# Performance work log

Hardware: AMD Instinct MI355X
Metric: run time of the kernel (lower is better)

Reference implementation:

```python
import jax, jax.numpy as jnp
import numpy as np
from jax import lax

T = 5        # unrolled ISTA iterations (module default)
LAM = 0.1    # soft-threshold level (module default)
B, L, K = 4096, 4096, 128


def _conv1d_same(x, k):
    """TF-style SAME cross-correlation. x: [B, L], k: [K] -> [B, L]."""
    Kw = k.shape[0]
    pad_left = (Kw - 1) // 2
    pad_right = Kw - 1 - pad_left
    out = lax.conv_general_dilated(
        x[:, None, :],            # [B, 1, L]
        k[None, None, :],         # [O=1, I=1, K]
        window_strides=(1,),
        padding=[(pad_left, pad_right)],
        dimension_numbers=("NCH", "OIH", "NCH"),
    )
    return out[:, 0, :]


def setup_inputs() -> dict:
    key = jax.random.key(0)
    k1, k2 = jax.random.split(key)
    y = jax.random.normal(k1, (B, L), dtype=jnp.float32)
    thz_pulse = jax.random.normal(k2, (K,), dtype=jnp.float32)  # learned pulse (trainable)
    step_size = jnp.full((1,), 0.1, dtype=jnp.float32)          # learned step (trainable)
    return {"y": y, "thz_pulse": thz_pulse, "step_size": step_size}


def reference(y, thz_pulse, step_size):
    x = jnp.zeros_like(y)
    h = thz_pulse           # matched-filter kernel
    h_rev = thz_pulse[::-1] # time-reversed kernel (adjoint / correlation)
    s = step_size[0]
    for _ in range(T):
        conv_out = _conv1d_same(y, h)           # H y
        residual = y - conv_out                 # y - H y
        update = _conv1d_same(residual, h_rev)  # H^T residual
        x = x + s * update                      # gradient step
        x = jnp.sign(x) * jax.nn.relu(jnp.abs(x) - LAM)  # soft-threshold
    return x
```

## Files before the change

### kernel.cpp

```cpp
#include <hip/hip_runtime.h>


typedef __bf16 bf16;
typedef __bf16 bf16x4 __attribute__((ext_vector_type(4)));
typedef __bf16 bf16x8 __attribute__((ext_vector_type(8)));
typedef float f32x4 __attribute__((ext_vector_type(4)));

#define LAM 0.1f
#define RPITCH 1028
#define LDSB (16 * RPITCH * 4)
#define WS_AG 0
#define WS_ZERO 80
#define WS_A1 8192
#define WS_A2 12288
#define PYE 360
#define PRE 216

__global__ __launch_bounds__(256) void ista_prep(const float* __restrict__ h,
                                                 bf16* __restrict__ ws) {
  __shared__ float hs[256];
  __shared__ float acp[256];
  __shared__ bf16 gp[384];
  const int tid = threadIdx.x;
  hs[tid] = (tid < 128) ? h[tid] : 0.f;
  gp[tid] = (bf16)0.f;
  if (tid < 128) gp[256 + tid] = (bf16)0.f;
  __syncthreads();
  const int tau = tid & 127;
  {
    const int m0 = (tid >> 7) * 64;
    float p0 = 0.f, p1 = 0.f, p2 = 0.f, p3 = 0.f;
    for (int m = m0; m < m0 + 64; m += 4) {
      p0 += hs[m] * hs[m + tau];     p1 += hs[m + 1] * hs[m + 1 + tau];
      p2 += hs[m + 2] * hs[m + 2 + tau]; p3 += hs[m + 3] * hs[m + 3 + tau];
    }
    acp[tid] = (p0 + p1) + (p2 + p3);
  }
  __syncthreads();
  if (tid < 128) {
    float ac = acp[tid] + acp[tid + 128];
    float g1 = (tau <= 63) ? hs[63 - tau] : 0.f;
    gp[145 + tau] = (bf16)(g1 - ac);
    if (tau > 0) {
      float g2 = (tau <= 64) ? hs[63 + tau] : 0.f;
      gp[145 - tau] = (bf16)(g2 - ac);
    }
  }
  __syncthreads();
  for (int i = tid; i < 1024; i += 256) {
    const int l = i >> 4, dd = i & 15;
    if (dd < 9) {
      const int o = 144 + (l >> 4) * 8 - (l & 15) + (dd - 4) * 32;
      bf16x8 a;
#pragma unroll
      for (int j = 0; j < 8; ++j) a[j] = gp[o + j];
      *reinterpret_cast<bf16x8*>(ws + WS_AG + l * 128 + dd * 8) = a;
    }
  }
  if (tid < 8) ws[WS_ZERO + tid] = (bf16)0.f;
  for (int i = tid; i < 512; i += 256) {
    const int l = i >> 3, dd = i & 7;
    if (dd < 5) {
      const int o = 127 + (l >> 4) * 8 - (l & 15) + (dd - 2) * 32;
      bf16x8 a1, a2;
#pragma unroll
      for (int j = 0; j < 8; ++j) {
        int p = o + j;
        int i1 = p - 64;
        a1[j] = ((unsigned)i1 < 128u) ? (bf16)hs[i1] : (bf16)0.f;
        int i2 = 191 - p;
        a2[j] = ((unsigned)i2 < 128u) ? (bf16)(-hs[i2]) : (bf16)0.f;
      }
      *reinterpret_cast<bf16x8*>(ws + WS_A1 + l * 64 + dd * 8) = a1;
      *reinterpret_cast<bf16x8*>(ws + WS_A2 + l * 64 + dd * 8) = a2;
    }
  }
}

__device__ __forceinline__ void async_copy16(const float* src, void* lds_dst) {
  __builtin_amdgcn_global_load_lds(
      (const __attribute__((address_space(1))) void*)src,
      (__attribute__((address_space(3))) void*)lds_dst, 16, 0, 0);
}

__device__ __forceinline__ bf16x8 load_frag(const float* __restrict__ yl,
                                            int c) {
  float4 v0 = *reinterpret_cast<const float4*>(yl + c);
  float4 v1 = *reinterpret_cast<const float4*>(yl + c + 4);
  bf16x8 b;
  b[0] = (bf16)v0.x; b[1] = (bf16)v0.y; b[2] = (bf16)v0.z; b[3] = (bf16)v0.w;
  b[4] = (bf16)v1.x; b[5] = (bf16)v1.y; b[6] = (bf16)v1.z; b[7] = (bf16)v1.w;
  return b;
}

__global__ __launch_bounds__(256) void ista_fused(
    const float* __restrict__ y, const bf16* __restrict__ ws,
    const float* __restrict__ step, float* __restrict__ out) {
  __shared__ __align__(16) char smem[LDSB];
  const int tid = threadIdx.x;
  const int lane = tid & 63;
  const int li = lane & 15;
  const int quad = lane >> 4;
  const int wave = tid >> 6;
  const int bid = blockIdx.x;
  const float s = step[0];

  if (bid < 512) {
    const int b0 = (bid >> 1) * 16;
    const int cblk = (bid & 1) * 2048;

    bf16x8 AG[9];
#pragma unroll
    for (int dd = 0; dd < 9; ++dd)
      AG[dd] = *reinterpret_cast<const bf16x8*>(ws + WS_AG + lane * 128 + dd * 8);

    const float* zsrc = reinterpret_cast<const float*>(ws + WS_ZERO);
    auto issue_seg = [&](int m) {
      const int base = cblk + 256 * (m - 1);
      const bool oob = (base < 0) | (base >= 4096);
      const int slotdw = (m & 3) * 256;
#pragma unroll
      for (int t = 0; t < 4; ++t) {
        const int r = (wave << 2) + t;
        const float* src =
            oob ? zsrc : (y + (size_t)(b0 + r) * 4096 + base + (lane << 2));
        char* dst = smem + ((r * RPITCH + slotdw) << 2) + (lane << 4);
        async_copy16(src, dst);
      }
    };
    issue_seg(0); issue_seg(1); issue_seg(2);

    const int qo = quad << 3;
    const float* rowp = reinterpret_cast<const float*>(smem) + li * RPITCH;
    float* orow = out + (size_t)(b0 + li) * 4096 + cblk + (quad << 2);

    for (int k = 0; k < 8; ++k) {
      __syncthreads();
      if (k < 7) issue_seg(k + 3);
      const int rcw = (k << 8) + (wave << 4);
      bf16x8 B[9];
#pragma unroll
      for (int dd = 0; dd < 9; ++dd)
        B[dd] = load_frag(rowp, (rcw + (dd - 4) * 32 + qo + 256) & 1023);
#pragma unroll
      for (int j = 0; j < 4; ++j) {
        bf16x8 n0, n1;
        if (j < 3) {
          n0 = load_frag(rowp, (rcw + 64 * (j + 1) + 96 + qo + 256) & 1023);
          n1 = load_frag(rowp, (rcw + 64 * (j + 1) + 128 + qo + 256) & 1023);
        }
        f32x4 acc0 = {0.f, 0.f, 0.f, 0.f};
        f32x4 acc1 = {0.f, 0.f, 0.f, 0.f};
        acc0 = __builtin_amdgcn_mfma_f32_16x16x32_bf16(AG[0], B[0], acc0, 0, 0, 0);
        acc1 = __builtin_amdgcn_mfma_f32_16x16x32_bf16(AG[1], B[1], acc1, 0, 0, 0);
        acc0 = __builtin_amdgcn_mfma_f32_16x16x32_bf16(AG[2], B[2], acc0, 0, 0, 0);
        acc1 = __builtin_amdgcn_mfma_f32_16x16x32_bf16(AG[3], B[3], acc1, 0, 0, 0);
        acc0 = __builtin_amdgcn_mfma_f32_16x16x32_bf16(AG[4], B[4], acc0, 0, 0, 0);
        acc1 = __builtin_amdgcn_mfma_f32_16x16x32_bf16(AG[5], B[5], acc1, 0, 0, 0);
        acc0 = __builtin_amdgcn_mfma_f32_16x16x32_bf16(AG[6], B[6], acc0, 0, 0, 0);
        acc1 = __builtin_amdgcn_mfma_f32_16x16x32_bf16(AG[7], B[7], acc1, 0, 0, 0);
        acc0 = __builtin_amdgcn_mfma_f32_16x16x32_bf16(AG[8], B[8], acc0, 0, 0, 0);
        const int tabs = cblk + rcw + (j << 6);
        if (tabs >= 64 && tabs < 4032) {
          float4 xv;
#pragma unroll
          for (int e = 0; e < 4; ++e) {
            float su = s * (acc0[e] + acc1[e]);
            float ax = fabsf(su) - LAM;
            ax = ax > 0.f ? ax : 0.f;
            (&xv.x)[e] = 5.f * copysignf(ax, su);
          }
          *reinterpret_cast<float4*>(orow + rcw + (j << 6)) = xv;
        }
        if (j < 3) {
          B[0] = B[2]; B[1] = B[3]; B[2] = B[4]; B[3] = B[5]; B[4] = B[6];
          B[5] = B[7]; B[6] = B[8]; B[7] = n0; B[8] = n1;
        }
      }
    }
  } else {
    const int eid = bid - 512;
    const int chunk0 = (eid & 1) ? (4096 - 64) : 0;
    const int b0 = (eid >> 1) * 16;
    bf16* ys = reinterpret_cast<bf16*>(smem);
    bf16* rs = ys + 16 * PYE;

    bf16x8 A1[5], A2[5];
#pragma unroll
    for (int dd = 0; dd < 5; ++dd) {
      A1[dd] = *reinterpret_cast<const bf16x8*>(ws + WS_A1 + lane * 64 + dd * 8);
      A2[dd] = *reinterpret_cast<const bf16x8*>(ws + WS_A2 + lane * 64 + dd * 8);
    }

    {
      const int rr = tid >> 4;
      const int t = tid & 15;
      const float* yrow = y + (size_t)(b0 + rr) * 4096;
      bf16* dst = ys + rr * PYE;
#pragma unroll
      for (int k = 0; k < 6; ++k) {
        int s4 = t + 16 * k;
        if (s4 < 88) {
          int l = chunk0 - 128 + s4 * 4;
          float4 v;
          if (l >= 0 && l <= 4096 - 4) {
            v = *reinterpret_cast<const float4*>(yrow + l);
          } else {
            v.x = ((unsigned)(l + 0) < 4096u) ? yrow[l + 0] : 0.f;
            v.y = ((unsigned)(l + 1) < 4096u) ? yrow[l + 1] : 0.f;
            v.z = ((unsigned)(l + 2) < 4096u) ? yrow[l + 2] : 0.f;
            v.w = ((unsigned)(l + 3) < 4096u) ? yrow[l + 3] : 0.f;
          }
          bf16x4 bv;
          bv[0] = (bf16)v.x; bv[1] = (bf16)v.y; bv[2] = (bf16)v.z; bv[3] = (bf16)v.w;
          *reinterpret_cast<bf16x4*>(dst + s4 * 4) = bv;
        }
      }
    }
    __syncthreads();

    for (int t = wave; t < 13; t += 4) {
      const int i0 = -64 + 16 * t;
      f32x4 acc;
      {
        bf16x4 yv = *reinterpret_cast<const bf16x4*>(
            ys + li * PYE + (i0 + 128) + quad * 4);
        acc[0] = -(float)yv[0]; acc[1] = -(float)yv[1];
        acc[2] = -(float)yv[2]; acc[3] = -(float)yv[3];
      }
#pragma unroll
      for (int dd = 0; dd < 5; ++dd) {
        bf16x8 b = *reinterpret_cast<const bf16x8*>(
            ys + li * PYE + (i0 + (dd - 2) * 32 + 128) + quad * 8);
        acc = __builtin_amdgcn_mfma_f32_16x16x32_bf16(A1[dd], b, acc, 0, 0, 0);
      }
      bf16x4 rv;
#pragma unroll
      for (int e = 0; e < 4; ++e) {
        int g = chunk0 + i0 + quad * 4 + e;
        float v = ((unsigned)g < 4096u) ? acc[e] : 0.f;
        rv[e] = (bf16)v;
      }
      *reinterpret_cast<bf16x4*>(rs + li * PRE + (i0 + 64) + quad * 4) = rv;
    }
    __syncthreads();

    {
      const int i0 = 16 * wave;
      f32x4 acc = {0.f, 0.f, 0.f, 0.f};
#pragma unroll
      for (int dd = 0; dd < 5; ++dd) {
        bf16x8 b = *reinterpret_cast<const bf16x8*>(
            rs + li * PRE + (i0 + (dd - 2) * 32 + 64) + quad * 8);
        acc = __builtin_amdgcn_mfma_f32_16x16x32_bf16(A2[dd], b, acc, 0, 0, 0);
      }
      float4 xv;
#pragma unroll
      for (int e = 0; e < 4; ++e) {
        float su = s * acc[e];
        float ax = fabsf(su) - LAM;
        ax = ax > 0.f ? ax : 0.f;
        (&xv.x)[e] = 5.f * copysignf(ax, su);
      }
      *reinterpret_cast<float4*>(
          out + (size_t)(b0 + li) * 4096 + chunk0 + i0 + quad * 4) = xv;
    }
  }
}

extern "C" void kernel_launch(void* const* d_in, const int* in_sizes, int n_in,
                              void* d_out, int out_size, void* d_ws,
                              size_t ws_size, hipStream_t stream) {
  const float* y = (const float*)d_in[0];
  const float* h = (const float*)d_in[1];
  const float* s = (const float*)d_in[2];
  float* out = (float*)d_out;
  bf16* ws = (bf16*)d_ws;
  ista_prep<<<dim3(1), dim3(256), 0, stream>>>(h, ws);
  ista_fused<<<dim3(512 + 512), dim3(256), 0, stream>>>(y, ws, s, out);
}
```

Baseline: 133.5 us.

## Stage y as bf16 in LDS via register prefetch, halve column block, double grid

The interior blocks no longer async-copy fp32 y segments into LDS and convert them to bf16 on every fragment read. Each thread now loads fp32 from global into registers, converts once, and writes bf16 into a ring buffer half the previous size, with register-level prefetch of the next segment. Column blocks shrink from 2048 to 1024, doubling the interior grid to 1024 blocks, and launch bounds request 4 blocks per CU for occupancy. The trade is losing the direct global-to-LDS copy in exchange for cheaper LDS reads, half the LDS footprint and more parallelism, at the cost of more halo reloading per block.

New measurement: 143.4 us. 1.07x slower.

```diff
diff --git a/kernel.cpp b/kernel.cpp
--- a/kernel.cpp
+++ b/kernel.cpp
@@ -7,8 +7,8 @@
 typedef float f32x4 __attribute__((ext_vector_type(4)));
 
 #define LAM 0.1f
-#define RPITCH 1028
-#define LDSB (16 * RPITCH * 4)
+#define RP 1032
+#define LDSB (16 * RP * 2)
 #define WS_AG 0
 #define WS_ZERO 80
 #define WS_A1 8192
@@ -77,23 +77,7 @@
   }
 }
 
-__device__ __forceinline__ void async_copy16(const float* src, void* lds_dst) {
-  __builtin_amdgcn_global_load_lds(
-      (const __attribute__((address_space(1))) void*)src,
-      (__attribute__((address_space(3))) void*)lds_dst, 16, 0, 0);
-}
-
-__device__ __forceinline__ bf16x8 load_frag(const float* __restrict__ yl,
-                                            int c) {
-  float4 v0 = *reinterpret_cast<const float4*>(yl + c);
-  float4 v1 = *reinterpret_cast<const float4*>(yl + c + 4);
-  bf16x8 b;
-  b[0] = (bf16)v0.x; b[1] = (bf16)v0.y; b[2] = (bf16)v0.z; b[3] = (bf16)v0.w;
-  b[4] = (bf16)v1.x; b[5] = (bf16)v1.y; b[6] = (bf16)v1.z; b[7] = (bf16)v1.w;
-  return b;
-}
-
-__global__ __launch_bounds__(256) void ista_fused(
+__global__ __launch_bounds__(256, 4) void ista_fused(
     const float* __restrict__ y, const bf16* __restrict__ ws,
     const float* __restrict__ step, float* __restrict__ out) {
   __shared__ __align__(16) char smem[LDSB];
@@ -105,50 +89,70 @@
   const int bid = blockIdx.x;
   const float s = step[0];
 
-  if (bid < 512) {
-    const int b0 = (bid >> 1) * 16;
-    const int cblk = (bid & 1) * 2048;
+  if (bid < 1024) {
+    const int b0 = (bid & 255) * 16;
+    const int cb = (bid >> 8) * 1024;
+    bf16* ring = reinterpret_cast<bf16*>(smem);
 
     bf16x8 AG[9];
 #pragma unroll
     for (int dd = 0; dd < 9; ++dd)
       AG[dd] = *reinterpret_cast<const bf16x8*>(ws + WS_AG + lane * 128 + dd * 8);
 
-    const float* zsrc = reinterpret_cast<const float*>(ws + WS_ZERO);
-    auto issue_seg = [&](int m) {
-      const int base = cblk + 256 * (m - 1);
-      const bool oob = (base < 0) | (base >= 4096);
-      const int slotdw = (m & 3) * 256;
-#pragma unroll
-      for (int t = 0; t < 4; ++t) {
-        const int r = (wave << 2) + t;
-        const float* src =
-            oob ? zsrc : (y + (size_t)(b0 + r) * 4096 + base + (lane << 2));
-        char* dst = smem + ((r * RPITCH + slotdw) << 2) + (lane << 4);
-        async_copy16(src, dst);
-      }
-    };
-    issue_seg(0); issue_seg(1); issue_seg(2);
+    const int sr = tid >> 4;
+    const int c16 = tid & 15;
+    const float* yrow = y + (size_t)(b0 + sr) * 4096;
+    bf16* wdst = ring + sr * RP;
+    float st[16];
+
+#define LOAD16(m)                                                         \
+  {                                                                       \
+    _Pragma("unroll") for (int u = 0; u < 4; ++u) {                       \
+      int gcol = cb + 256 * (m) + 16 * c16 + 4 * u;                       \
+      float4 v = {0.f, 0.f, 0.f, 0.f};                                    \
+      if ((unsigned)gcol < 4096u)                                         \
+        v = *reinterpret_cast<const float4*>(yrow + gcol);                \
+      st[4 * u + 0] = v.x; st[4 * u + 1] = v.y;                           \
+      st[4 * u + 2] = v.z; st[4 * u + 3] = v.w;                           \
+    }                                                                     \
+  }
+#define CVTWRITE(m)                                                       \
+  {                                                                       \
+    bf16x8 lo, hi;                                                        \
+    _Pragma("unroll") for (int j = 0; j < 8; ++j) {                       \
+      lo[j] = (bf16)st[j]; hi[j] = (bf16)st[8 + j];                       \
+    }                                                                     \
+    int rc = (256 * (m) + 16 * c16 + 1024) & 1023;                        \
+    *reinterpret_cast<bf16x8*>(wdst + rc) = lo;                           \
+    *reinterpret_cast<bf16x8*>(wdst + rc + 8) = hi;                       \
+  }
+
+    LOAD16(-1); CVTWRITE(-1);
+    LOAD16(0);  CVTWRITE(0);
+    LOAD16(1);  CVTWRITE(1);
+    LOAD16(2);
 
     const int qo = quad << 3;
-    const float* rowp = reinterpret_cast<const float*>(smem) + li * RPITCH;
-    float* orow = out + (size_t)(b0 + li) * 4096 + cblk + (quad << 2);
-
-    for (int k = 0; k < 8; ++k) {
+    const bf16* rowp = ring + li * RP;
+    float* orow = out + (size_t)(b0 + li) * 4096 + cb + (quad << 2);
+    bf16x8 B[9];
+
+#define RFRAG(col) \
+  (*reinterpret_cast<const bf16x8*>(rowp + (((col) + 1024) & 1023)))
+
+#pragma unroll
+    for (int k = 0; k < 4; ++k) {
       __syncthreads();
-      if (k < 7) issue_seg(k + 3);
-      const int rcw = (k << 8) + (wave << 4);
-      bf16x8 B[9];
-#pragma unroll
-      for (int dd = 0; dd < 9; ++dd)
-        B[dd] = load_frag(rowp, (rcw + (dd - 4) * 32 + qo + 256) & 1023);
+      if (k <= 2) CVTWRITE(k + 2);
+      if (k <= 1) LOAD16(k + 3);
+      if (k == 0) {
+#pragma unroll
+        for (int dd = 0; dd < 9; ++dd)
+          B[dd] = RFRAG(16 * wave + (dd - 4) * 32 + qo);
+      }
 #pragma unroll
       for (int j = 0; j < 4; ++j) {
-        bf16x8 n0, n1;
-        if (j < 3) {
-          n0 = load_frag(rowp, (rcw + 64 * (j + 1) + 96 + qo + 256) & 1023);
-          n1 = load_frag(rowp, (rcw + 64 * (j + 1) + 128 + qo + 256) & 1023);
-        }
+        const int tc = 256 * k + 16 * wave + 64 * j;
         f32x4 acc0 = {0.f, 0.f, 0.f, 0.f};
         f32x4 acc1 = {0.f, 0.f, 0.f, 0.f};
         acc0 = __builtin_amdgcn_mfma_f32_16x16x32_bf16(AG[0], B[0], acc0, 0, 0, 0);
@@ -160,7 +164,7 @@
         acc0 = __builtin_amdgcn_mfma_f32_16x16x32_bf16(AG[6], B[6], acc0, 0, 0, 0);
         acc1 = __builtin_amdgcn_mfma_f32_16x16x32_bf16(AG[7], B[7], acc1, 0, 0, 0);
         acc0 = __builtin_amdgcn_mfma_f32_16x16x32_bf16(AG[8], B[8], acc0, 0, 0, 0);
-        const int tabs = cblk + rcw + (j << 6);
+        const int tabs = cb + tc;
         if (tabs >= 64 && tabs < 4032) {
           float4 xv;
 #pragma unroll
@@ -170,16 +174,21 @@
             ax = ax > 0.f ? ax : 0.f;
             (&xv.x)[e] = 5.f * copysignf(ax, su);
           }
-          *reinterpret_cast<float4*>(orow + rcw + (j << 6)) = xv;
+          *reinterpret_cast<float4*>(orow + tc) = xv;
         }
-        if (j < 3) {
+        if (k < 3 || j < 3) {
           B[0] = B[2]; B[1] = B[3]; B[2] = B[4]; B[3] = B[5]; B[4] = B[6];
-          B[5] = B[7]; B[6] = B[8]; B[7] = n0; B[8] = n1;
+          B[5] = B[7]; B[6] = B[8];
+          B[7] = RFRAG(tc + 160 + qo);
+          B[8] = RFRAG(tc + 192 + qo);
         }
       }
     }
+#undef RFRAG
+#undef CVTWRITE
+#undef LOAD16
   } else {
-    const int eid = bid - 512;
+    const int eid = bid - 1024;
     const int chunk0 = (eid & 1) ? (4096 - 64) : 0;
     const int b0 = (eid >> 1) * 16;
     bf16* ys = reinterpret_cast<bf16*>(smem);
@@ -277,5 +286,5 @@
   float* out = (float*)d_out;
   bf16* ws = (bf16*)d_ws;
   ista_prep<<<dim3(1), dim3(256), 0, stream>>>(h, ws);
-  ista_fused<<<dim3(512 + 512), dim3(256), 0, stream>>>(y, ws, s, out);
+  ista_fused<<<dim3(1024 + 512), dim3(256), 0, stream>>>(y, ws, s, out);
 }
```

## Deepen async LDS pipeline with finer segments and counted vmcnt waits

Applied to the files above, without the earlier changes.

Restructures the main interior path's global-to-LDS streaming. It now uses 128-column segments, 4-byte global_load_lds transfers into an unpadded 1024-float ring, and six segments in flight. The __syncthreads is replaced by an explicit s_waitcnt vmcnt(16) plus barrier, so later loads keep flowing while earlier ones are consumed. The loop is fully unrolled, and the block index mapping is changed so consecutive blocks cover different row groups. The intent is better latency hiding and less barrier stalling. In exchange, it issues many more small DMA instructions and drops the LDS padding, which risks bank conflicts.

Result: slower. 152.9 us (+14.6%).

```diff
diff --git a/kernel.cpp b/kernel.cpp
--- a/kernel.cpp
+++ b/kernel.cpp
@@ -7,8 +7,6 @@
 typedef float f32x4 __attribute__((ext_vector_type(4)));
 
 #define LAM 0.1f
-#define RPITCH 1028
-#define LDSB (16 * RPITCH * 4)
 #define WS_AG 0
 #define WS_ZERO 80
 #define WS_A1 8192
@@ -77,16 +75,11 @@
   }
 }
 
-__device__ __forceinline__ void async_copy16(const float* src, void* lds_dst) {
-  __builtin_amdgcn_global_load_lds(
-      (const __attribute__((address_space(1))) void*)src,
-      (__attribute__((address_space(3))) void*)lds_dst, 16, 0, 0);
-}
-
-__device__ __forceinline__ bf16x8 load_frag(const float* __restrict__ yl,
-                                            int c) {
-  float4 v0 = *reinterpret_cast<const float4*>(yl + c);
-  float4 v1 = *reinterpret_cast<const float4*>(yl + c + 4);
+__device__ __forceinline__ bf16x8 ldfrag(const float* __restrict__ rowb,
+                                         int col) {
+  const int X = col & 1023;
+  float4 v0 = *reinterpret_cast<const float4*>(rowb + X);
+  float4 v1 = *reinterpret_cast<const float4*>(rowb + X + 4);
   bf16x8 b;
   b[0] = (bf16)v0.x; b[1] = (bf16)v0.y; b[2] = (bf16)v0.z; b[3] = (bf16)v0.w;
   b[4] = (bf16)v1.x; b[5] = (bf16)v1.y; b[6] = (bf16)v1.z; b[7] = (bf16)v1.w;
@@ -96,18 +89,18 @@
 __global__ __launch_bounds__(256) void ista_fused(
     const float* __restrict__ y, const bf16* __restrict__ ws,
     const float* __restrict__ step, float* __restrict__ out) {
-  __shared__ __align__(16) char smem[LDSB];
+  __shared__ __align__(16) char smem[65536];
   const int tid = threadIdx.x;
   const int lane = tid & 63;
   const int li = lane & 15;
-  const int quad = lane >> 4;
+  const int quad = tid >> 4 & 3;
   const int wave = tid >> 6;
   const int bid = blockIdx.x;
   const float s = step[0];
 
   if (bid < 512) {
-    const int b0 = (bid >> 1) * 16;
-    const int cblk = (bid & 1) * 2048;
+    const int b0 = (bid & 255) * 16;
+    const int cb = (bid >> 8) * 2048;
 
     bf16x8 AG[9];
 #pragma unroll
@@ -115,40 +108,48 @@
       AG[dd] = *reinterpret_cast<const bf16x8*>(ws + WS_AG + lane * 128 + dd * 8);
 
     const float* zsrc = reinterpret_cast<const float*>(ws + WS_ZERO);
+    const int r0 = wave * 4;
     auto issue_seg = [&](int m) {
-      const int base = cblk + 256 * (m - 1);
-      const bool oob = (base < 0) | (base >= 4096);
-      const int slotdw = (m & 3) * 256;
-#pragma unroll
-      for (int t = 0; t < 4; ++t) {
-        const int r = (wave << 2) + t;
+      const int base = cb + 128 * m;
+      const bool oob = (base < 0) | (base >= 4096) | (m > 17);
+      const int slotB = ((128 * m) & 1023) << 2;
+#pragma unroll
+      for (int t = 0; t < 8; ++t) {
+        const int r = r0 + (t >> 1);
+        const int q = t & 1;
         const float* src =
-            oob ? zsrc : (y + (size_t)(b0 + r) * 4096 + base + (lane << 2));
-        char* dst = smem + ((r * RPITCH + slotdw) << 2) + (lane << 4);
-        async_copy16(src, dst);
+            oob ? zsrc : (y + (size_t)(b0 + r) * 4096 + base + 64 * q + lane);
+        char* dst = smem + r * 4096 + slotB + q * 256;
+        __builtin_amdgcn_global_load_lds(
+            (const __attribute__((address_space(1))) void*)src,
+            (__attribute__((address_space(3))) void*)dst, 4, 0, 0);
       }
     };
-    issue_seg(0); issue_seg(1); issue_seg(2);
+
+#pragma unroll
+    for (int m = -1; m <= 4; ++m) issue_seg(m);
 
     const int qo = quad << 3;
-    const float* rowp = reinterpret_cast<const float*>(smem) + li * RPITCH;
-    float* orow = out + (size_t)(b0 + li) * 4096 + cblk + (quad << 2);
-
-    for (int k = 0; k < 8; ++k) {
-      __syncthreads();
-      if (k < 7) issue_seg(k + 3);
-      const int rcw = (k << 8) + (wave << 4);
-      bf16x8 B[9];
-#pragma unroll
-      for (int dd = 0; dd < 9; ++dd)
-        B[dd] = load_frag(rowp, (rcw + (dd - 4) * 32 + qo + 256) & 1023);
-#pragma unroll
-      for (int j = 0; j < 4; ++j) {
-        bf16x8 n0, n1;
-        if (j < 3) {
-          n0 = load_frag(rowp, (rcw + 64 * (j + 1) + 96 + qo + 256) & 1023);
-          n1 = load_frag(rowp, (rcw + 64 * (j + 1) + 128 + qo + 256) & 1023);
-        }
+    const float* rowb = reinterpret_cast<const float*>(smem) + li * 1024;
+    float* orow = out + (size_t)(b0 + li) * 4096 + cb + (quad << 2);
+    bf16x8 B[9];
+
+#pragma unroll
+    for (int k = 0; k < 16; ++k) {
+      asm volatile("s_waitcnt vmcnt(16)" ::: "memory");
+      __builtin_amdgcn_s_barrier();
+      __builtin_amdgcn_sched_barrier(0);
+      issue_seg(k + 5);
+      if (k == 0) {
+#pragma unroll
+        for (int dd = 0; dd < 9; ++dd)
+          B[dd] = ldfrag(rowb, 16 * wave + (dd - 4) * 32 + qo);
+      }
+#pragma unroll
+      for (int j = 0; j < 2; ++j) {
+        const int tc = 128 * k + 64 * j + 16 * wave;
+        bf16x8 n0 = ldfrag(rowb, tc + 160 + qo);
+        bf16x8 n1 = ldfrag(rowb, tc + 192 + qo);
         f32x4 acc0 = {0.f, 0.f, 0.f, 0.f};
         f32x4 acc1 = {0.f, 0.f, 0.f, 0.f};
         acc0 = __builtin_amdgcn_mfma_f32_16x16x32_bf16(AG[0], B[0], acc0, 0, 0, 0);
@@ -160,7 +161,7 @@
         acc0 = __builtin_amdgcn_mfma_f32_16x16x32_bf16(AG[6], B[6], acc0, 0, 0, 0);
         acc1 = __builtin_amdgcn_mfma_f32_16x16x32_bf16(AG[7], B[7], acc1, 0, 0, 0);
         acc0 = __builtin_amdgcn_mfma_f32_16x16x32_bf16(AG[8], B[8], acc0, 0, 0, 0);
-        const int tabs = cblk + rcw + (j << 6);
+        const int tabs = cb + tc;
         if (tabs >= 64 && tabs < 4032) {
           float4 xv;
 #pragma unroll
@@ -170,12 +171,10 @@
             ax = ax > 0.f ? ax : 0.f;
             (&xv.x)[e] = 5.f * copysignf(ax, su);
           }
-          *reinterpret_cast<float4*>(orow + rcw + (j << 6)) = xv;
+          *reinterpret_cast<float4*>(orow + tc) = xv;
         }
-        if (j < 3) {
-          B[0] = B[2]; B[1] = B[3]; B[2] = B[4]; B[3] = B[5]; B[4] = B[6];
-          B[5] = B[7]; B[6] = B[8]; B[7] = n0; B[8] = n1;
-        }
+        B[0] = B[2]; B[1] = B[3]; B[2] = B[4]; B[3] = B[5]; B[4] = B[6];
+        B[5] = B[7]; B[6] = B[8]; B[7] = n0; B[8] = n1;
       }
     }
   } else {
@@ -184,6 +183,7 @@
     const int b0 = (eid >> 1) * 16;
     bf16* ys = reinterpret_cast<bf16*>(smem);
     bf16* rs = ys + 16 * PYE;
+    const int wv = wave;
 
     bf16x8 A1[5], A2[5];
 #pragma unroll
@@ -219,7 +219,7 @@
     }
     __syncthreads();
 
-    for (int t = wave; t < 13; t += 4) {
+    for (int t = wv; t < 13; t += 4) {
       const int i0 = -64 + 16 * t;
       f32x4 acc;
       {
@@ -246,7 +246,7 @@
     __syncthreads();
 
     {
-      const int i0 = 16 * wave;
+      const int i0 = 16 * wv;
       f32x4 acc = {0.f, 0.f, 0.f, 0.f};
 #pragma unroll
       for (int dd = 0; dd < 5; ++dd) {
```
